# Kernel optimization log

Measured on AMD Instinct MI355X. Metric: run time of the kernel, lower is better.

## Reference

```python
import jax, jax.numpy as jnp
import numpy as np
from jax import lax

CONF_THRES = 0.2
IOU_THRES = 0.4
MAX_DET = 10
TOPK = 5


def _iou_matrix(b):
    # b: [N,4] (x1,y1,x2,y2) -> [N,N] pairwise IoU
    area = jnp.clip(b[:, 2] - b[:, 0], 0) * jnp.clip(b[:, 3] - b[:, 1], 0)
    lt = jnp.maximum(b[:, None, :2], b[None, :, :2])
    rb = jnp.minimum(b[:, None, 2:], b[None, :, 2:])
    wh = jnp.clip(rb - lt, 0)
    inter = wh[..., 0] * wh[..., 1]
    return inter / (area[:, None] + area[None, :] - inter + 1e-9)


def _nms_single(boxes):
    # boxes: [N,5]; greedy NMS with fixed MAX_DET iterations (jit-static)
    conf = boxes[:, 4]
    pass_t = conf > CONF_THRES
    use_thres = jnp.any(pass_t)
    cand0 = jnp.where(use_thres, pass_t, jnp.ones_like(pass_t))
    ious = _iou_matrix(boxes[:, :4])

    def step(cand, _):
        scores = jnp.where(cand, conf, -jnp.inf)
        idx = jnp.argmax(scores)
        has = scores[idx] > -jnp.inf
        sup = ious[idx] > IOU_THRES
        new_cand = (cand & ~sup).at[idx].set(False)
        new_cand = jnp.where(has, new_cand, cand)
        return new_cand, (idx, has)

    _, (idxs, valid) = lax.scan(step, cand0, None, length=MAX_DET)
    kept = boxes[idxs]  # [MAX_DET,5]
    # tiny_filter: drop boxes with w<1 or h<1
    valid = valid & ((kept[:, 2] - kept[:, 0]) >= 1) & ((kept[:, 3] - kept[:, 1]) >= 1)
    # fallback branch keeps only boxes[:topk]
    valid = valid & jnp.where(use_thres, True, jnp.arange(MAX_DET) < TOPK)
    return kept, valid


def _forward(x, region_boxes, W_sem, b_sem, W1, b1, W2, b2, W3, b3):
    B, C, H, W = x.shape
    D = W_sem.shape[1]
    # semantic feature map (semantic_estab modeled as learned 1x1 projection)
    seman = jnp.einsum('bchw,cd->bhwd', x, W_sem) + b_sem  # [B,H,W,D]
    # per-image NMS + tiny filter (region_boxes is detached in the original)
    kept, valid = jax.vmap(_nms_single)(lax.stop_gradient(region_boxes))
    # round box coords like (box + 0.5).to(int), clip to image
    xi = jnp.floor(kept[..., :4] + 0.5).astype(jnp.int32)
    x1 = jnp.clip(xi[..., 0], 0, W)
    y1 = jnp.clip(xi[..., 1], 0, H)
    x2 = jnp.clip(xi[..., 2], 0, W)
    y2 = jnp.clip(xi[..., 3], 0, H)
    xx = jnp.arange(W)
    yy = jnp.arange(H)
    inside = ((xx[None, None, None, :] >= x1[:, :, None, None])
              & (xx[None, None, None, :] < x2[:, :, None, None])
              & (yy[None, None, :, None] >= y1[:, :, None, None])
              & (yy[None, None, :, None] < y2[:, :, None, None])
              & valid[:, :, None, None])  # [B,MAX_DET,H,W]
    inside_any = jnp.any(inside, axis=1)  # [B,H,W]
    mask_maps = ~inside_any  # True = background (as in original mask_maps)
    # scatter region semantic features into the word tensor; positions outside
    # any box are padding (zeros), matching region_words_pad semantics
    words = jnp.where(inside_any[..., None], seman, 0.0).reshape(B, H * W, D)
    # transformer is identity here; pro_embed MLP (3 layers, relu on first two)
    h1 = jax.nn.relu(words @ W1 + b1)
    h2 = jax.nn.relu(h1 @ W2 + b2)
    seg = h2 @ W3 + b3[:1]  # [B,HW,1]
    seg_output = jnp.transpose(seg, (1, 0, 2))  # output.permute(1,0,2)
    return seg_output, mask_maps, kept, valid


def setup_inputs() -> dict:
    key = jax.random.key(0)
    ks = jax.random.split(key, 12)
    B, C, H, W, D, N = 4, 64, 128, 128, 256, 100
    x = jax.random.normal(ks[0], (B, C, H, W), dtype=jnp.float32)
    # structured proposal boxes: centers inside image, sizes 2..16, conf in [0,1]
    cx = jax.random.uniform(ks[1], (B, N), minval=10.0, maxval=W - 10.0)
    cy = jax.random.uniform(ks[2], (B, N), minval=10.0, maxval=H - 10.0)
    bw = jax.random.uniform(ks[3], (B, N), minval=1.0, maxval=8.0)
    bh = jax.random.uniform(ks[4], (B, N), minval=1.0, maxval=8.0)
    conf = jax.random.uniform(ks[5], (B, N))
    region_boxes = jnp.stack([cx - bw, cy - bh, cx + bw, cy + bh, conf], axis=-1)
    s = 1.0 / np.sqrt(D)
    return {
        'x': x,
        'region_boxes': region_boxes,
        'W_sem': jax.random.normal(ks[6], (C, D), dtype=jnp.float32) / np.sqrt(C),
        'b_sem': jnp.zeros((D,), jnp.float32),
        'W1': jax.random.normal(ks[7], (D, D), dtype=jnp.float32) * s,
        'b1': jnp.zeros((D,), jnp.float32),
        'W2': jax.random.normal(ks[8], (D, D), dtype=jnp.float32) * s,
        'b2': jnp.zeros((D,), jnp.float32),
        'W3': jax.random.normal(ks[9], (D, 1), dtype=jnp.float32) * s,
        'b3': jnp.zeros((D,), jnp.float32),
    }


def reference(x, region_boxes, W_sem, b_sem, W1, b1, W2, b2, W3, b3):
    return _forward(x, region_boxes, W_sem, b_sem, W1, b1, W2, b2, W3, b3)
```

## Files before the change

kernel.cpp:

```cpp
#include <hip/hip_runtime.h>

typedef __attribute__((ext_vector_type(8))) short bf16x8;
typedef __attribute__((ext_vector_type(4))) float f32x4;

#define BB 4
#define CCH 64
#define HH 128
#define WW 128
#define DD 256
#define NBOX 100
#define MAXDET 10
#define TOPK 5

#define SEG_OFF   0
#define MASK_OFF  (BB * HH * WW)
#define KEPT_OFF  (MASK_OFF + BB * HH * WW)
#define VALID_OFF (KEPT_OFF + BB * MAXDET * 5)

#define WS_CNTB 0
#define WS_SEG0 8
#define WS_BITS 16
#define WS_LIST (WS_BITS + 4096)
#define WB_BYTE_OFF 131072
#define WB_SEM 0
#define WB_W1  (32 * 512)
#define WB_W2  (160 * 512)

__device__ __forceinline__ unsigned short f2bf(float f) {
    unsigned u = __float_as_uint(f);
    u = (u + 0x7FFFu + ((u >> 16) & 1u)) >> 16;
    return (unsigned short)u;
}
__device__ __forceinline__ float bf2f(unsigned short s) {
    return __uint_as_float(((unsigned)s) << 16);
}

__global__ __launch_bounds__(256) void k1_kernel(
    const float* __restrict__ rb,
    const float* __restrict__ Wsem, const float* __restrict__ W1,
    const float* __restrict__ W2,
    const float* __restrict__ b1,   const float* __restrict__ b2,
    const float* __restrict__ W3,   const float* __restrict__ b3,
    float* __restrict__ out, int* __restrict__ wsI,
    float* __restrict__ wsF, short* __restrict__ wb)
{
    const int bid = blockIdx.x;
    const int t   = threadIdx.x;

    if (bid < BB) {
        __shared__ float lb[NBOX * 5];
        __shared__ int   rectsS[MAXDET * 4];
        __shared__ int   valdS[MAXDET];
        __shared__ int   sc[256];

        for (int k = t; k < NBOX * 5; k += 256) lb[k] = rb[bid * NBOX * 5 + k];
        __syncthreads();

        if (t < 64) {
            const float b0x1 = lb[t*5], b0y1 = lb[t*5+1], b0x2 = lb[t*5+2],
                        b0y2 = lb[t*5+3], b0c = lb[t*5+4];
            const bool has1 = t < (NBOX - 64);
            const int  j1 = t + 64;
            float c1x1=0.f, c1y1=0.f, c1x2=0.f, c1y2=0.f, c1c=-INFINITY;
            if (has1) { c1x1=lb[j1*5]; c1y1=lb[j1*5+1]; c1x2=lb[j1*5+2];
                        c1y2=lb[j1*5+3]; c1c=lb[j1*5+4]; }
            const float a0 = fmaxf(b0x2-b0x1,0.f)*fmaxf(b0y2-b0y1,0.f);
            const float a1 = fmaxf(c1x2-c1x1,0.f)*fmaxf(c1y2-c1y1,0.f);

            unsigned long long bal = __ballot(b0c > 0.2f) | __ballot(has1 && (c1c > 0.2f));
            const bool use_thres = (bal != 0ULL);
            bool cand0 = use_thres ? (b0c > 0.2f) : true;
            bool cand1 = has1 && (use_thres ? (c1c > 0.2f) : true);

            for (int det = 0; det < MAXDET; ++det) {
                float v  = cand0 ? b0c : -INFINITY;
                int  idx = t;
                if (cand1 && c1c > v) { v = c1c; idx = j1; }
                for (int off = 1; off < 64; off <<= 1) {
                    float v2 = __shfl_xor(v, off);
                    int   i2 = __shfl_xor(idx, off);
                    if (v2 > v || (v2 == v && i2 < idx)) { v = v2; idx = i2; }
                }
                const bool has = (v > -INFINITY);
                const float sx1 = lb[idx*5], sy1 = lb[idx*5+1], sx2 = lb[idx*5+2],
                            sy2 = lb[idx*5+3], sc5 = lb[idx*5+4];
                if (has) {
                    const float sa = fmaxf(sx2-sx1,0.f)*fmaxf(sy2-sy1,0.f);
                    {
                        float lx=fmaxf(sx1,b0x1), ly=fmaxf(sy1,b0y1);
                        float rx=fminf(sx2,b0x2), ry=fminf(sy2,b0y2);
                        float inter=fmaxf(rx-lx,0.f)*fmaxf(ry-ly,0.f);
                        if (inter/(sa + a0 - inter + 1e-9f) > 0.4f) cand0 = false;
                    }
                    if (has1) {
                        float lx=fmaxf(sx1,c1x1), ly=fmaxf(sy1,c1y1);
                        float rx=fminf(sx2,c1x2), ry=fminf(sy2,c1y2);
                        float inter=fmaxf(rx-lx,0.f)*fmaxf(ry-ly,0.f);
                        if (inter/(sa + a1 - inter + 1e-9f) > 0.4f) cand1 = false;
                    }
                    if (idx == t)  cand0 = false;
                    if (idx == j1) cand1 = false;
                }
                if (t == 0) {
                    float* kp = out + KEPT_OFF + (bid*MAXDET + det)*5;
                    kp[0]=sx1; kp[1]=sy1; kp[2]=sx2; kp[3]=sy2; kp[4]=sc5;
                    const int vld = (has && (sx2-sx1 >= 1.f) && (sy2-sy1 >= 1.f) &&
                                     (use_thres || det < TOPK)) ? 1 : 0;
                    out[VALID_OFF + bid*MAXDET + det] = vld ? 1.f : 0.f;
                    int x1 = min(max((int)floorf(sx1+0.5f),0),WW);
                    int y1 = min(max((int)floorf(sy1+0.5f),0),HH);
                    int x2 = min(max((int)floorf(sx2+0.5f),0),WW);
                    int y2 = min(max((int)floorf(sy2+0.5f),0),HH);
                    rectsS[det*4]=x1; rectsS[det*4+1]=y1;
                    rectsS[det*4+2]=x2; rectsS[det*4+3]=y2;
                    valdS[det] = vld;
                }
            }
        }
        __syncthreads();

        int myBits[4];
        int n = 0;
        #pragma unroll
        for (int k = 0; k < 4; ++k) {
            const int s = t*4 + k;
            const int h = s >> 3, w0 = (s & 7) << 4;
            unsigned bits = 0;
            for (int d = 0; d < MAXDET; ++d) {
                if (valdS[d] && h >= rectsS[d*4+1] && h < rectsS[d*4+3]) {
                    const int lo = max(rectsS[d*4],   w0);
                    const int hi = min(rectsS[d*4+2], w0 + 16);
                    if (lo < hi) bits |= ((1u << (hi - w0)) - (1u << (lo - w0)));
                }
            }
            myBits[k] = (int)bits;
            n += __popc(bits);
            wsI[WS_BITS + bid*1024 + s] = (int)bits;
            float* mp = out + MASK_OFF + bid*(HH*WW) + s*16;
            #pragma unroll
            for (int q = 0; q < 4; ++q) {
                float4 v;
                v.x = ((bits >> (q*4+0)) & 1) ? 0.f : 1.f;
                v.y = ((bits >> (q*4+1)) & 1) ? 0.f : 1.f;
                v.z = ((bits >> (q*4+2)) & 1) ? 0.f : 1.f;
                v.w = ((bits >> (q*4+3)) & 1) ? 0.f : 1.f;
                *reinterpret_cast<float4*>(mp + q*4) = v;
            }
        }
        sc[t] = n;
        __syncthreads();
        for (int off = 1; off < 256; off <<= 1) {
            const int v = (t >= off) ? sc[t - off] : 0;
            __syncthreads();
            sc[t] += v;
            __syncthreads();
        }
        if (t == 255) wsI[WS_CNTB + bid] = sc[255];
        int pos = sc[t] - n;
        #pragma unroll
        for (int k = 0; k < 4; ++k) {
            unsigned bitsr = (unsigned)myBits[k];
            const int s = t*4 + k;
            while (bitsr) {
                const int bp = __ffs(bitsr) - 1;
                bitsr &= bitsr - 1;
                wsI[WS_LIST + bid*4096 + pos++] = s*16 + bp;
            }
        }
    } else if (bid == BB) {
        __shared__ float h1s[DD];
        __shared__ float red[DD];
        h1s[t] = fmaxf(b1[t], 0.f);
        __syncthreads();
        float acc = b2[t];
        for (int i = 0; i < DD; ++i) acc = fmaf(h1s[i], W2[i*DD + t], acc);
        red[t] = fmaxf(acc, 0.f) * W3[t];
        __syncthreads();
        for (int off = 128; off > 0; off >>= 1) {
            if (t < off) red[t] += red[t + off];
            __syncthreads();
        }
        if (t == 0) wsF[WS_SEG0] = red[0] + b3[0];
    } else {
        const int g = (bid - BB - 1) * 4 + (t >> 6);
        const int l = t & 63;
        const float* src; int KK32, cp, sbase;
        if (g < 32)       { src = Wsem; KK32 = 2; cp = g;       sbase = WB_SEM; }
        else if (g < 160) { src = W1;   KK32 = 8; cp = g - 32;  sbase = WB_W1; }
        else              { src = W2;   KK32 = 8; cp = g - 160; sbase = WB_W2; }
        const int wq  = cp / (4 * KK32);
        const int rem = cp % (4 * KK32);
        const int nt = rem / KK32, kk = rem % KK32;
        const int k0 = kk*32 + (l >> 4)*8;
        const int nn = wq*64 + nt*16 + (l & 15);
        unsigned short h[8];
        #pragma unroll
        for (int j = 0; j < 8; ++j) h[j] = f2bf(src[(size_t)(k0 + j) * DD + nn]);
        int4 v;
        v.x = (int)((unsigned)h[0] | ((unsigned)h[1] << 16));
        v.y = (int)((unsigned)h[2] | ((unsigned)h[3] << 16));
        v.z = (int)((unsigned)h[4] | ((unsigned)h[5] << 16));
        v.w = (int)((unsigned)h[6] | ((unsigned)h[7] << 16));
        *reinterpret_cast<int4*>(wb + sbase + (size_t)cp*512 + l*8) = v;
    }
}

__global__ __launch_bounds__(256) void k2_kernel(
    const float* __restrict__ x,
    const float* __restrict__ bsem, const float* __restrict__ b1,
    const float* __restrict__ b2,   const float* __restrict__ W3,
    const float* __restrict__ b3,
    const int* __restrict__ wsI, const float* __restrict__ wsF,
    const short* __restrict__ wb, float* __restrict__ out)
{
    const int bi = blockIdx.x;
    const int t  = threadIdx.x;

    if (bi >= 1024) {
        const int px = (bi - 1024) * 256 + t;
        const int b = px >> 14, hw = px & 16383;
        const unsigned bits = (unsigned)wsI[WS_BITS + b*1024 + (hw >> 4)];
        if (!((bits >> (hw & 15)) & 1)) out[SEG_OFF + hw*BB + b] = wsF[WS_SEG0];
        return;
    }

    const int b    = bi >> 8;
    const int base = (bi & 255) << 4;
    const int cntb = wsI[WS_CNTB + b];
    if (base >= cntb) return;

    __shared__ short actX[16 * 80];
    __shared__ short actA[16 * 264];
    __shared__ short actB[16 * 264];
    __shared__ int   recs[16];

    if (t < 16) {
        const int id = base + t;
        recs[t] = (id < cntb) ? wsI[WS_LIST + b*4096 + id] : -1;
    }
    __syncthreads();

    {
        const int p = t & 15, cg = t >> 4;
        int hw = recs[p]; if (hw < 0) hw = recs[0];
        const float* xp = x + ((size_t)b * CCH) * (HH * WW) + hw;
        #pragma unroll
        for (int i = 0; i < 4; ++i) {
            const int c = cg*4 + i;
            actX[p*80 + c] = (short)f2bf(xp[(size_t)c * (HH * WW)]);
        }
    }
    __syncthreads();

    const int w = t >> 6, l = t & 63;
    const int lm = l & 15, lg = l >> 4;
    f32x4 acc[4];

    #pragma unroll
    for (int nt = 0; nt < 4; ++nt) acc[nt] = f32x4{0.f, 0.f, 0.f, 0.f};
    #pragma unroll
    for (int kk = 0; kk < 2; ++kk) {
        const bf16x8 av = *reinterpret_cast<const bf16x8*>(&actX[lm*80 + kk*32 + lg*8]);
        #pragma unroll
        for (int nt = 0; nt < 4; ++nt) {
            const bf16x8 bv = *reinterpret_cast<const bf16x8*>(
                wb + WB_SEM + (size_t)((w*4 + nt)*2 + kk)*512 + l*8);
            acc[nt] = __builtin_amdgcn_mfma_f32_16x16x32_bf16(av, bv, acc[nt], 0, 0, 0);
        }
    }
    #pragma unroll
    for (int nt = 0; nt < 4; ++nt) {
        const int n = w*64 + nt*16 + lm;
        const float bias = bsem[n];
        #pragma unroll
        for (int r = 0; r < 4; ++r)
            actA[(lg*4 + r)*264 + n] = (short)f2bf(acc[nt][r] + bias);
    }
    __syncthreads();

    #pragma unroll
    for (int nt = 0; nt < 4; ++nt) acc[nt] = f32x4{0.f, 0.f, 0.f, 0.f};
    #pragma unroll
    for (int kk = 0; kk < 8; ++kk) {
        const bf16x8 av = *reinterpret_cast<const bf16x8*>(&actA[lm*264 + kk*32 + lg*8]);
        #pragma unroll
        for (int nt = 0; nt < 4; ++nt) {
            const bf16x8 bv = *reinterpret_cast<const bf16x8*>(
                wb + WB_W1 + (size_t)((w*4 + nt)*8 + kk)*512 + l*8);
            acc[nt] = __builtin_amdgcn_mfma_f32_16x16x32_bf16(av, bv, acc[nt], 0, 0, 0);
        }
    }
    #pragma unroll
    for (int nt = 0; nt < 4; ++nt) {
        const int n = w*64 + nt*16 + lm;
        const float bias = b1[n];
        #pragma unroll
        for (int r = 0; r < 4; ++r)
            actB[(lg*4 + r)*264 + n] = (short)f2bf(fmaxf(acc[nt][r] + bias, 0.f));
    }
    __syncthreads();

    #pragma unroll
    for (int nt = 0; nt < 4; ++nt) acc[nt] = f32x4{0.f, 0.f, 0.f, 0.f};
    #pragma unroll
    for (int kk = 0; kk < 8; ++kk) {
        const bf16x8 av = *reinterpret_cast<const bf16x8*>(&actB[lm*264 + kk*32 + lg*8]);
        #pragma unroll
        for (int nt = 0; nt < 4; ++nt) {
            const bf16x8 bv = *reinterpret_cast<const bf16x8*>(
                wb + WB_W2 + (size_t)((w*4 + nt)*8 + kk)*512 + l*8);
            acc[nt] = __builtin_amdgcn_mfma_f32_16x16x32_bf16(av, bv, acc[nt], 0, 0, 0);
        }
    }
    #pragma unroll
    for (int nt = 0; nt < 4; ++nt) {
        const int n = w*64 + nt*16 + lm;
        const float bias = b2[n];
        #pragma unroll
        for (int r = 0; r < 4; ++r)
            actA[(lg*4 + r)*264 + n] = (short)f2bf(fmaxf(acc[nt][r] + bias, 0.f));
    }
    __syncthreads();

    const float w3v0 = W3[l], w3v1 = W3[l + 64], w3v2 = W3[l + 128], w3v3 = W3[l + 192];
    #pragma unroll
    for (int q = 0; q < 4; ++q) {
        const int p = w*4 + q;
        float v = bf2f((unsigned short)actA[p*264 + l])       * w3v0
                + bf2f((unsigned short)actA[p*264 + l + 64])  * w3v1
                + bf2f((unsigned short)actA[p*264 + l + 128]) * w3v2
                + bf2f((unsigned short)actA[p*264 + l + 192]) * w3v3;
        #pragma unroll
        for (int off = 32; off > 0; off >>= 1) v += __shfl_down(v, off);
        if (l == 0) {
            const int hw = recs[p];
            if (hw >= 0) out[SEG_OFF + hw*BB + b] = v + b3[0];
        }
    }
}

extern "C" void kernel_launch(void* const* d_in, const int* in_sizes, int n_in,
                              void* d_out, int out_size, void* d_ws, size_t ws_size,
                              hipStream_t stream) {
    const float* x    = (const float*)d_in[0];
    const float* rb   = (const float*)d_in[1];
    const float* Wsem = (const float*)d_in[2];
    const float* bsem = (const float*)d_in[3];
    const float* W1   = (const float*)d_in[4];
    const float* b1   = (const float*)d_in[5];
    const float* W2   = (const float*)d_in[6];
    const float* b2   = (const float*)d_in[7];
    const float* W3   = (const float*)d_in[8];
    const float* b3   = (const float*)d_in[9];
    float* out = (float*)d_out;
    int*   wsI = (int*)d_ws;
    float* wsF = (float*)d_ws;
    short* wb  = (short*)((char*)d_ws + WB_BYTE_OFF);

    k1_kernel<<<BB + 1 + 72, 256, 0, stream>>>(rb, Wsem, W1, W2, b1, b2, W3, b3,
                                               out, wsI, wsF, wb);
    k2_kernel<<<1280, 256, 0, stream>>>(x, bsem, b1, b2, W3, b3, wsI, wsF, wb, out);
}
```

Baseline: 105.7 us.

## Persistent MLP blocks and batch-interleaved bitmask for vectorized fill

The MLP part of k2 now runs on a fixed grid of 256 blocks, 64 per image, each looping over its image's masked-pixel list in strides, instead of launching 1024 blocks that mostly exit early. The bitmask is stored interleaved by batch, so each fill thread reads all four images' bits with one int4 load and writes a float4 to the [hw,B] output, cutting the fill grid to 64 blocks. The intent is to cut launch and idle-block overhead and make fill stores coalesced. The cost is less parallelism when masks are large, plus an unroll pragma on the small bias-MLP loop.

Result: faster. 99.99 us (-5.4%).

```diff
diff --git a/kernel.cpp b/kernel.cpp
--- a/kernel.cpp
+++ b/kernel.cpp
@@ -25,6 +25,9 @@
 #define WB_SEM 0
 #define WB_W1  (32 * 512)
 #define WB_W2  (160 * 512)
+
+#define NMLP  256
+#define NFILL 64
 
 __device__ __forceinline__ unsigned short f2bf(float f) {
     unsigned u = __float_as_uint(f);
@@ -135,7 +138,7 @@
             }
             myBits[k] = (int)bits;
             n += __popc(bits);
-            wsI[WS_BITS + bid*1024 + s] = (int)bits;
+            wsI[WS_BITS + s*4 + bid] = (int)bits;
             float* mp = out + MASK_OFF + bid*(HH*WW) + s*16;
             #pragma unroll
             for (int q = 0; q < 4; ++q) {
@@ -173,6 +176,7 @@
         h1s[t] = fmaxf(b1[t], 0.f);
         __syncthreads();
         float acc = b2[t];
+        #pragma unroll 8
         for (int i = 0; i < DD; ++i) acc = fmaf(h1s[i], W2[i*DD + t], acc);
         red[t] = fmaxf(acc, 0.f) * W3[t];
         __syncthreads();
@@ -216,125 +220,142 @@
     const int bi = blockIdx.x;
     const int t  = threadIdx.x;
 
-    if (bi >= 1024) {
-        const int px = (bi - 1024) * 256 + t;
-        const int b = px >> 14, hw = px & 16383;
-        const unsigned bits = (unsigned)wsI[WS_BITS + b*1024 + (hw >> 4)];
-        if (!((bits >> (hw & 15)) & 1)) out[SEG_OFF + hw*BB + b] = wsF[WS_SEG0];
+    if (bi >= NMLP) {
+        const int hw  = (bi - NMLP) * 256 + t;
+        const int s   = hw >> 4, bit = hw & 15;
+        const int4 bw = *reinterpret_cast<const int4*>(wsI + WS_BITS + s*4);
+        const float s0 = wsF[WS_SEG0];
+        const unsigned i0 = (((unsigned)bw.x) >> bit) & 1u;
+        const unsigned i1 = (((unsigned)bw.y) >> bit) & 1u;
+        const unsigned i2 = (((unsigned)bw.z) >> bit) & 1u;
+        const unsigned i3 = (((unsigned)bw.w) >> bit) & 1u;
+        float* op = out + SEG_OFF + hw * 4;
+        if (!(i0 | i1 | i2 | i3)) {
+            float4 v; v.x = s0; v.y = s0; v.z = s0; v.w = s0;
+            *reinterpret_cast<float4*>(op) = v;
+        } else {
+            if (!i0) op[0] = s0;
+            if (!i1) op[1] = s0;
+            if (!i2) op[2] = s0;
+            if (!i3) op[3] = s0;
+        }
         return;
     }
 
-    const int b    = bi >> 8;
-    const int base = (bi & 255) << 4;
+    const int b    = bi >> 6;
+    const int blk  = bi & 63;
     const int cntb = wsI[WS_CNTB + b];
-    if (base >= cntb) return;
 
     __shared__ short actX[16 * 80];
     __shared__ short actA[16 * 264];
     __shared__ short actB[16 * 264];
     __shared__ int   recs[16];
 
-    if (t < 16) {
-        const int id = base + t;
-        recs[t] = (id < cntb) ? wsI[WS_LIST + b*4096 + id] : -1;
-    }
-    __syncthreads();
-
-    {
-        const int p = t & 15, cg = t >> 4;
-        int hw = recs[p]; if (hw < 0) hw = recs[0];
-        const float* xp = x + ((size_t)b * CCH) * (HH * WW) + hw;
-        #pragma unroll
-        for (int i = 0; i < 4; ++i) {
-            const int c = cg*4 + i;
-            actX[p*80 + c] = (short)f2bf(xp[(size_t)c * (HH * WW)]);
-        }
-    }
-    __syncthreads();
-
     const int w = t >> 6, l = t & 63;
     const int lm = l & 15, lg = l >> 4;
-    f32x4 acc[4];
-
-    #pragma unroll
-    for (int nt = 0; nt < 4; ++nt) acc[nt] = f32x4{0.f, 0.f, 0.f, 0.f};
-    #pragma unroll
-    for (int kk = 0; kk < 2; ++kk) {
-        const bf16x8 av = *reinterpret_cast<const bf16x8*>(&actX[lm*80 + kk*32 + lg*8]);
+
+    for (int base = blk * 16; base < cntb; base += NMLP / BB * 16) {
+        __syncthreads();
+        if (t < 16) {
+            const int id = base + t;
+            recs[t] = (id < cntb) ? wsI[WS_LIST + b*4096 + id] : -1;
+        }
+        __syncthreads();
+
+        {
+            const int p = t & 15, cg = t >> 4;
+            int hw = recs[p]; if (hw < 0) hw = recs[0];
+            const float* xp = x + ((size_t)b * CCH) * (HH * WW) + hw;
+            #pragma unroll
+            for (int i = 0; i < 4; ++i) {
+                const int c = cg*4 + i;
+                actX[p*80 + c] = (short)f2bf(xp[(size_t)c * (HH * WW)]);
+            }
+        }
+        __syncthreads();
+
+        f32x4 acc[4];
+
+        #pragma unroll
+        for (int nt = 0; nt < 4; ++nt) acc[nt] = f32x4{0.f, 0.f, 0.f, 0.f};
+        #pragma unroll
+        for (int kk = 0; kk < 2; ++kk) {
+            const bf16x8 av = *reinterpret_cast<const bf16x8*>(&actX[lm*80 + kk*32 + lg*8]);
+            #pragma unroll
+            for (int nt = 0; nt < 4; ++nt) {
+                const bf16x8 bv = *reinterpret_cast<const bf16x8*>(
+                    wb + WB_SEM + (size_t)((w*4 + nt)*2 + kk)*512 + l*8);
+                acc[nt] = __builtin_amdgcn_mfma_f32_16x16x32_bf16(av, bv, acc[nt], 0, 0, 0);
+            }
+        }
         #pragma unroll
         for (int nt = 0; nt < 4; ++nt) {
-            const bf16x8 bv = *reinterpret_cast<const bf16x8*>(
-                wb + WB_SEM + (size_t)((w*4 + nt)*2 + kk)*512 + l*8);
-            acc[nt] = __builtin_amdgcn_mfma_f32_16x16x32_bf16(av, bv, acc[nt], 0, 0, 0);
-        }
-    }
-    #pragma unroll
-    for (int nt = 0; nt < 4; ++nt) {
-        const int n = w*64 + nt*16 + lm;
-        const float bias = bsem[n];
-        #pragma unroll
-        for (int r = 0; r < 4; ++r)
-            actA[(lg*4 + r)*264 + n] = (short)f2bf(acc[nt][r] + bias);
-    }
-    __syncthreads();
-
-    #pragma unroll
-    for (int nt = 0; nt < 4; ++nt) acc[nt] = f32x4{0.f, 0.f, 0.f, 0.f};
-    #pragma unroll
-    for (int kk = 0; kk < 8; ++kk) {
-        const bf16x8 av = *reinterpret_cast<const bf16x8*>(&actA[lm*264 + kk*32 + lg*8]);
+            const int n = w*64 + nt*16 + lm;
+            const float bias = bsem[n];
+            #pragma unroll
+            for (int r = 0; r < 4; ++r)
+                actA[(lg*4 + r)*264 + n] = (short)f2bf(acc[nt][r] + bias);
+        }
+        __syncthreads();
+
+        #pragma unroll
+        for (int nt = 0; nt < 4; ++nt) acc[nt] = f32x4{0.f, 0.f, 0.f, 0.f};
+        #pragma unroll
+        for (int kk = 0; kk < 8; ++kk) {
+            const bf16x8 av = *reinterpret_cast<const bf16x8*>(&actA[lm*264 + kk*32 + lg*8]);
+            #pragma unroll
+            for (int nt = 0; nt < 4; ++nt) {
+                const bf16x8 bv = *reinterpret_cast<const bf16x8*>(
+                    wb + WB_W1 + (size_t)((w*4 + nt)*8 + kk)*512 + l*8);
+                acc[nt] = __builtin_amdgcn_mfma_f32_16x16x32_bf16(av, bv, acc[nt], 0, 0, 0);
+            }
+        }
         #pragma unroll
         for (int nt = 0; nt < 4; ++nt) {
-            const bf16x8 bv = *reinterpret_cast<const bf16x8*>(
-                wb + WB_W1 + (size_t)((w*4 + nt)*8 + kk)*512 + l*8);
-            acc[nt] = __builtin_amdgcn_mfma_f32_16x16x32_bf16(av, bv, acc[nt], 0, 0, 0);
-        }
-    }
-    #pragma unroll
-    for (int nt = 0; nt < 4; ++nt) {
-        const int n = w*64 + nt*16 + lm;
-        const float bias = b1[n];
-        #pragma unroll
-        for (int r = 0; r < 4; ++r)
-            actB[(lg*4 + r)*264 + n] = (short)f2bf(fmaxf(acc[nt][r] + bias, 0.f));
-    }
-    __syncthreads();
-
-    #pragma unroll
-    for (int nt = 0; nt < 4; ++nt) acc[nt] = f32x4{0.f, 0.f, 0.f, 0.f};
-    #pragma unroll
-    for (int kk = 0; kk < 8; ++kk) {
-        const bf16x8 av = *reinterpret_cast<const bf16x8*>(&actB[lm*264 + kk*32 + lg*8]);
+            const int n = w*64 + nt*16 + lm;
+            const float bias = b1[n];
+            #pragma unroll
+            for (int r = 0; r < 4; ++r)
+                actB[(lg*4 + r)*264 + n] = (short)f2bf(fmaxf(acc[nt][r] + bias, 0.f));
+        }
+        __syncthreads();
+
+        #pragma unroll
+        for (int nt = 0; nt < 4; ++nt) acc[nt] = f32x4{0.f, 0.f, 0.f, 0.f};
+        #pragma unroll
+        for (int kk = 0; kk < 8; ++kk) {
+            const bf16x8 av = *reinterpret_cast<const bf16x8*>(&actB[lm*264 + kk*32 + lg*8]);
+            #pragma unroll
+            for (int nt = 0; nt < 4; ++nt) {
+                const bf16x8 bv = *reinterpret_cast<const bf16x8*>(
+                    wb + WB_W2 + (size_t)((w*4 + nt)*8 + kk)*512 + l*8);
+                acc[nt] = __builtin_amdgcn_mfma_f32_16x16x32_bf16(av, bv, acc[nt], 0, 0, 0);
+            }
+        }
         #pragma unroll
         for (int nt = 0; nt < 4; ++nt) {
-            const bf16x8 bv = *reinterpret_cast<const bf16x8*>(
-                wb + WB_W2 + (size_t)((w*4 + nt)*8 + kk)*512 + l*8);
-            acc[nt] = __builtin_amdgcn_mfma_f32_16x16x32_bf16(av, bv, acc[nt], 0, 0, 0);
-        }
-    }
-    #pragma unroll
-    for (int nt = 0; nt < 4; ++nt) {
-        const int n = w*64 + nt*16 + lm;
-        const float bias = b2[n];
-        #pragma unroll
-        for (int r = 0; r < 4; ++r)
-            actA[(lg*4 + r)*264 + n] = (short)f2bf(fmaxf(acc[nt][r] + bias, 0.f));
-    }
-    __syncthreads();
-
-    const float w3v0 = W3[l], w3v1 = W3[l + 64], w3v2 = W3[l + 128], w3v3 = W3[l + 192];
-    #pragma unroll
-    for (int q = 0; q < 4; ++q) {
-        const int p = w*4 + q;
-        float v = bf2f((unsigned short)actA[p*264 + l])       * w3v0
-                + bf2f((unsigned short)actA[p*264 + l + 64])  * w3v1
-                + bf2f((unsigned short)actA[p*264 + l + 128]) * w3v2
-                + bf2f((unsigned short)actA[p*264 + l + 192]) * w3v3;
-        #pragma unroll
-        for (int off = 32; off > 0; off >>= 1) v += __shfl_down(v, off);
-        if (l == 0) {
-            const int hw = recs[p];
-            if (hw >= 0) out[SEG_OFF + hw*BB + b] = v + b3[0];
+            const int n = w*64 + nt*16 + lm;
+            const float bias = b2[n];
+            #pragma unroll
+            for (int r = 0; r < 4; ++r)
+                actA[(lg*4 + r)*264 + n] = (short)f2bf(fmaxf(acc[nt][r] + bias, 0.f));
+        }
+        __syncthreads();
+
+        const float w3v0 = W3[l], w3v1 = W3[l + 64], w3v2 = W3[l + 128], w3v3 = W3[l + 192];
+        #pragma unroll
+        for (int q = 0; q < 4; ++q) {
+            const int p = w*4 + q;
+            float v = bf2f((unsigned short)actA[p*264 + l])       * w3v0
+                    + bf2f((unsigned short)actA[p*264 + l + 64])  * w3v1
+                    + bf2f((unsigned short)actA[p*264 + l + 128]) * w3v2
+                    + bf2f((unsigned short)actA[p*264 + l + 192]) * w3v3;
+            #pragma unroll
+            for (int off = 32; off > 0; off >>= 1) v += __shfl_down(v, off);
+            if (l == 0) {
+                const int hw = recs[p];
+                if (hw >= 0) out[SEG_OFF + hw*4 + b] = v + b3[0];
+            }
         }
     }
 }
@@ -359,5 +380,6 @@
 
     k1_kernel<<<BB + 1 + 72, 256, 0, stream>>>(rb, Wsem, W1, W2, b1, b2, W3, b3,
                                                out, wsI, wsF, wb);
-    k2_kernel<<<1280, 256, 0, stream>>>(x, bsem, b1, b2, W3, b3, wsI, wsF, wb, out);
-}
+    k2_kernel<<<NMLP + NFILL, 256, 0, stream>>>(x, bsem, b1, b2, W3, b3,
+                                                wsI, wsF, wb, out);
+}
```
